# Kernel tuning notes

Measured on AMD Instinct MI355X. Metric: run time of the kernel, lower is better.

The kernel has to match this reference:

```python
import jax, jax.numpy as jnp
import numpy as np
from jax import lax

B, D, C, K = 8192, 512, 1000, 8
EPS = 1e-8
TEMP = 0.2
NEG = -10000.0


def setup_inputs() -> dict:
    key = jax.random.key(0)
    ks = jax.random.split(key, 6)
    z = jax.random.normal(ks[0], (B, D), dtype=jnp.float32)
    n_exp = jax.random.randint(ks[1], (B,), 0, K, dtype=jnp.int32)
    s1 = 1.0 / np.sqrt(D)
    W1 = jax.random.normal(ks[2], (K, D, D), dtype=jnp.float32) * s1
    b1 = jax.random.normal(ks[3], (K, D), dtype=jnp.float32) * 0.01
    W2 = jax.random.normal(ks[4], (K, D, C), dtype=jnp.float32) * s1
    b2 = jax.random.normal(ks[5], (K, C), dtype=jnp.float32) * 0.01
    return {"z": z, "n_exp": n_exp, "W1": W1, "b1": b1, "W2": W2, "b2": b2}


def _gates_one(p, c, n):
    # p: [K,C] softmax probs for one sample; c: [K] confidences; n: scalar int
    pn = p / (jnp.linalg.norm(p, axis=-1, keepdims=True) + EPS)
    S = pn @ pn.T  # [K,K] pairwise cosine similarity
    sel0 = jnp.zeros((K,), dtype=bool).at[jnp.argmax(c)].set(True)

    def body(t, sel):
        # max cosine sim of each candidate to already-selected set
        max_sim = jnp.max(jnp.where(sel[None, :], S, -jnp.inf), axis=1)
        dist = jnp.where(sel, -jnp.inf, 1.0 - max_sim)
        new = sel.at[jnp.argmax(dist)].set(True)
        return jnp.where(t < n, new, sel)

    sel = lax.fori_loop(1, K, body, sel0)
    gate_logits = jnp.where(sel, c, NEG) / TEMP
    return jax.nn.softmax(gate_logits)


def reference(z, n_exp, W1, b1, W2, b2):
    # K expert MLPs, batched: [B,d] -> [B,K,C]
    h = jax.nn.relu(jnp.einsum('bd,kde->bke', z, W1) + b1[None])
    logits_all = jnp.einsum('bke,kec->bkc', h, W2) + b2[None]
    probs = jax.nn.softmax(logits_all, axis=-1)
    conf = jnp.max(probs, axis=-1)  # [B,K]
    gates = jax.vmap(_gates_one)(probs, conf, n_exp)  # [B,K]
    logits = jnp.einsum('bkc,bk->bc', logits_all, gates)
    return logits, gates
```

## Files before the change

kernel.cpp:

```cpp
#include <hip/hip_runtime.h>
#include <math.h>

#define B_SZ 8192
#define D_DIM 512
#define C_DIM 1000
#define C_PAD 1024
#define K_EXP 8
#define TEMP_INV 5.0f
#define EPS_N 1e-8f

typedef __attribute__((ext_vector_type(8))) short frag_ab;
typedef __attribute__((ext_vector_type(16))) float f32x16;

__device__ __forceinline__ short f2bf(float f) {
    unsigned u = __builtin_bit_cast(unsigned, f);
    unsigned r = (u + 0x7fffu + ((u >> 16) & 1u)) >> 16;
    return (short)r;
}
__device__ __forceinline__ float bf2f(short s) {
    unsigned u = ((unsigned)(unsigned short)s) << 16;
    return __builtin_bit_cast(float, u);
}
__device__ __forceinline__ void split2(float v, short& s0, short& s1) {
    s0 = f2bf(v);
    s1 = f2bf(v - bf2f(s0));
}

__device__ __forceinline__ void gl_lds16(const short* g, short* l) {
    __builtin_amdgcn_global_load_lds(
        (const __attribute__((address_space(1))) unsigned int*)(const void*)g,
        (__attribute__((address_space(3))) unsigned int*)(void*)l,
        16, 0, 0);
}

__global__ __launch_bounds__(256) void prep_z(const float* __restrict__ z,
                                              short* __restrict__ p0, short* __restrict__ p1) {
    int idx = blockIdx.x * 256 + threadIdx.x;
    float v = z[idx];
    short a, b; split2(v, a, b);
    p0[idx] = a; p1[idx] = b;
}

__global__ __launch_bounds__(256) void prep_w1t(const float* __restrict__ W1,
                                                short* __restrict__ p0, short* __restrict__ p1) {
    __shared__ float t[32][33];
    const int k = blockIdx.z;
    const int d0 = blockIdx.x * 32;
    const int e0 = blockIdx.y * 32;
    const int tx = threadIdx.x & 31, ty = threadIdx.x >> 5;
    const float* src = W1 + ((size_t)k << 18);
#pragma unroll
    for (int r = 0; r < 4; r++) {
        int d = d0 + ty + 8 * r;
        t[ty + 8 * r][tx] = src[(size_t)d * 512 + e0 + tx];
    }
    __syncthreads();
#pragma unroll
    for (int r = 0; r < 4; r++) {
        int e = e0 + ty + 8 * r;
        int d = d0 + tx;
        float v = t[tx][ty + 8 * r];
        short a, b; split2(v, a, b);
        size_t o = ((size_t)k << 18) + (size_t)e * 512 + d;
        p0[o] = a; p1[o] = b;
    }
}

__global__ __launch_bounds__(256) void prep_w2t(const float* __restrict__ W2,
                                                short* __restrict__ p0, short* __restrict__ p1) {
    __shared__ float t[32][33];
    const int k = blockIdx.z;
    const int e0 = blockIdx.x * 32;
    const int c0 = blockIdx.y * 32;
    const int tx = threadIdx.x & 31, ty = threadIdx.x >> 5;
    const float* src = W2 + (size_t)k * (D_DIM * C_DIM);
#pragma unroll
    for (int r = 0; r < 4; r++) {
        int e = e0 + ty + 8 * r;
        int c = c0 + tx;
        t[ty + 8 * r][tx] = (c < C_DIM) ? src[(size_t)e * C_DIM + c] : 0.f;
    }
    __syncthreads();
#pragma unroll
    for (int r = 0; r < 4; r++) {
        int c = c0 + ty + 8 * r;
        int e = e0 + tx;
        float v = t[tx][ty + 8 * r];
        short a, b; split2(v, a, b);
        size_t o = (size_t)k * (C_PAD * D_DIM) + (size_t)c * 512 + e;
        p0[o] = a; p1[o] = b;
    }
}

__global__ __launch_bounds__(512, 2) void gemm_split(
    const short* __restrict__ A0, const short* __restrict__ A1, long long aBatch,
    const short* __restrict__ B0, const short* __restrict__ B1, long long bBatch,
    const float* __restrict__ bias, int biasBatch,
    float* __restrict__ Cf, long long cBatch, int ldc, int Nout,
    short* __restrict__ H0, short* __restrict__ H1, long long hBatch,
    int mt, int nt, int mode)
{
    const int lin = blockIdx.x;
    const int k = lin & 7;
    const int rem = lin >> 3;
    const int gm = (mt >= 2) ? 2 : 1;
    const int win = rem / (gm * nt);
    const int local = rem % (gm * nt);
    const int m0 = (win * gm + local / nt) * 256;
    const int n0 = (local % nt) * 256;

    const int tid = threadIdx.x;
    const int lane = tid & 63;
    const int wv = tid >> 6;
    const int wm = (wv & 1) * 128;
    const int wn = (wv >> 1) * 64;

    __shared__ short lds[65536];
    short* ldsA = lds;
    short* ldsB = lds + 32768;

    const short* aP0 = A0 + (size_t)k * aBatch + (size_t)m0 * 512;
    const short* aP1 = A1 + (size_t)k * aBatch + (size_t)m0 * 512;
    const short* bP0 = B0 + (size_t)k * bBatch + (size_t)n0 * 512;
    const short* bP1 = B1 + (size_t)k * bBatch + (size_t)n0 * 512;

    f32x16 acc[4][2];
#pragma unroll
    for (int i = 0; i < 4; i++)
#pragma unroll
        for (int j = 0; j < 2; j++)
            acc[i][j] = (f32x16)(0.f);

    const int srow = tid >> 2;
    const int sc   = tid & 3;
    const int khalf = lane >> 5;
    const int r31   = lane & 31;

#define SROW_STAGE(gsrc, ldst, KK0) do {                                        \
    _Pragma("unroll")                                                           \
    for (int hh = 0; hh < 2; hh++) {                                            \
        int row = hh * 128 + srow;                                              \
        int gq = sc ^ ((row >> 1) & 3);                                         \
        gl_lds16((gsrc) + (size_t)row * 512 + (KK0) + gq * 8,                   \
                 (ldst) + row * 32 + sc * 8);                                   \
    }                                                                           \
} while (0)

#define READ_B32(BUFC) do {                                                     \
    _Pragma("unroll")                                                           \
    for (int p = 0; p < 2; p++)                                                 \
        _Pragma("unroll")                                                       \
        for (int bj = 0; bj < 2; bj++) {                                        \
            int R = wn + bj * 32 + r31;                                         \
            _Pragma("unroll")                                                   \
            for (int kk = 0; kk < 2; kk++) {                                    \
                int ck = kk * 2 + khalf;                                        \
                int slot = ck ^ ((R >> 1) & 3);                                 \
                bfr[p][bj][kk] = *(const frag_ab*)(ldsB + (BUFC) + p * 8192 + R * 32 + slot * 8); \
            }                                                                   \
        }                                                                       \
} while (0)

#define READ_A32(DST, BLK, BUFC) do {                                           \
    int R = wm + (BLK) * 32 + r31;                                              \
    _Pragma("unroll")                                                           \
    for (int p = 0; p < 2; p++)                                                 \
        _Pragma("unroll")                                                       \
        for (int kk = 0; kk < 2; kk++) {                                        \
            int ck = kk * 2 + khalf;                                            \
            int slot = ck ^ ((R >> 1) & 3);                                     \
            DST[p][kk] = *(const frag_ab*)(ldsA + (BUFC) + p * 8192 + R * 32 + slot * 8); \
        }                                                                       \
} while (0)

#define MFMA_Q32(BLK, AR) do {                                                  \
    __builtin_amdgcn_s_setprio(1);                                              \
    _Pragma("unroll")                                                           \
    for (int bj = 0; bj < 2; bj++) {                                            \
        f32x16 c = acc[BLK][bj];                                                \
        _Pragma("unroll")                                                       \
        for (int kk = 0; kk < 2; kk++) {                                        \
            c = __builtin_amdgcn_mfma_f32_32x32x16_bf16(AR[0][kk], bfr[0][bj][kk], c, 0, 0, 0); \
            c = __builtin_amdgcn_mfma_f32_32x32x16_bf16(AR[0][kk], bfr[1][bj][kk], c, 0, 0, 0); \
            c = __builtin_amdgcn_mfma_f32_32x32x16_bf16(AR[1][kk], bfr[0][bj][kk], c, 0, 0, 0); \
        }                                                                       \
        acc[BLK][bj] = c;                                                       \
    }                                                                           \
    __builtin_amdgcn_s_setprio(0);                                              \
} while (0)

#define PH_BAR() do {                                                           \
    __builtin_amdgcn_sched_barrier(0);                                          \
    __builtin_amdgcn_s_barrier();                                               \
    __builtin_amdgcn_sched_barrier(0);                                          \
} while (0)

    SROW_STAGE(bP0, ldsB + 0,            0);
    SROW_STAGE(bP1, ldsB + 8192,         0);
    SROW_STAGE(aP0, ldsA + 0,            0);
    SROW_STAGE(aP1, ldsA + 8192,         0);
    SROW_STAGE(bP0, ldsB + 16384,        32);
    SROW_STAGE(bP1, ldsB + 16384 + 8192, 32);
    asm volatile("s_waitcnt vmcnt(4)" ::: "memory");
    PH_BAR();

    auto kstep = [&](int T, bool s01, bool s23, int vmn) __attribute__((always_inline)) {
        const int bufc = (T & 1) * 16384;
        const int nb1  = ((T + 1) & 1) * 16384;
        const int kk1  = (T + 1) * 32;
        const int kk2  = (T + 2) * 32;
        frag_ab bfr[2][2][2];
        frag_ab aC[2][2], aN[2][2];

        READ_B32(bufc);
        READ_A32(aC, 0, bufc);
        READ_A32(aN, 1, bufc);
        if (s01) SROW_STAGE(aP0, ldsA + nb1, kk1);
        MFMA_Q32(0, aC);
        PH_BAR();

        READ_A32(aC, 2, bufc);
        if (s01) SROW_STAGE(aP1, ldsA + nb1 + 8192, kk1);
        MFMA_Q32(1, aN);
        PH_BAR();

        READ_A32(aN, 3, bufc);
        if (s23) SROW_STAGE(bP0, ldsB + bufc, kk2);
        MFMA_Q32(2, aC);
        PH_BAR();

        if (s23) SROW_STAGE(bP1, ldsB + bufc + 8192, kk2);
        MFMA_Q32(3, aN);
        if (vmn == 4)      asm volatile("s_waitcnt vmcnt(4)" ::: "memory");
        else if (vmn == 0) asm volatile("s_waitcnt vmcnt(0)" ::: "memory");
        PH_BAR();
    };

    for (int t = 0; t < 14; ++t) kstep(t, true, true, 4);
    kstep(14, true, false, 0);
    kstep(15, false, false, -1);

#undef SROW_STAGE
#undef READ_B32
#undef READ_A32
#undef MFMA_Q32
#undef PH_BAR

    const int er0 = (lane >> 5) * 4;
    const int ec  = lane & 31;
    if (mode == 0) {
        float* C = Cf + (size_t)k * cBatch;
        const float* bb = bias + (size_t)k * biasBatch;
#pragma unroll
        for (int blk = 0; blk < 4; blk++) {
            int rowb = m0 + wm + blk * 32 + er0;
#pragma unroll
            for (int bj = 0; bj < 2; bj++) {
                int col = n0 + wn + bj * 32 + ec;
                if (col < Nout) {
                    float b = bb[col];
#pragma unroll
                    for (int rg = 0; rg < 16; rg++) {
                        int row = rowb + (rg & 3) + 8 * (rg >> 2);
                        C[(size_t)row * ldc + col] = acc[blk][bj][rg] + b;
                    }
                }
            }
        }
    } else {
        short* h0 = H0 + (size_t)k * hBatch;
        short* h1 = H1 + (size_t)k * hBatch;
        const float* bb = bias + (size_t)k * biasBatch;
#pragma unroll
        for (int blk = 0; blk < 4; blk++) {
            int rowb = m0 + wm + blk * 32 + er0;
#pragma unroll
            for (int bj = 0; bj < 2; bj++) {
                int col = n0 + wn + bj * 32 + ec;
                float b = bb[col];
#pragma unroll
                for (int rg = 0; rg < 16; rg++) {
                    int row = rowb + (rg & 3) + 8 * (rg >> 2);
                    float v = fmaxf(acc[blk][bj][rg] + b, 0.f);
                    short s0, s1; split2(v, s0, s1);
                    size_t o = (size_t)row * 512 + col;
                    h0[o] = s0; h1[o] = s1;
                }
            }
        }
    }
}

__global__ __launch_bounds__(256) void gate_combine(
    const float* __restrict__ L,
    const int* __restrict__ n_exp,
    float* __restrict__ out_logits,
    float* __restrict__ out_gates,
    int Bc)
{
    const int wv = threadIdx.x >> 6;
    const int lane = threadIdx.x & 63;
    const int b = blockIdx.x * 4 + wv;
    const size_t kcs = (size_t)Bc * C_DIM;
    const float* Lb = L + (size_t)b * C_DIM;

    __shared__ float Sm[4][64];
    __shared__ float Zm[4][8];

    float mx[K_EXP], Zs[K_EXP], dd[36];
#pragma unroll
    for (int k = 0; k < K_EXP; k++) { mx[k] = -INFINITY; Zs[k] = 0.f; }
#pragma unroll
    for (int p = 0; p < 36; p++) dd[p] = 0.f;

    for (int c = lane; c < C_DIM; c += 64) {
        float e[K_EXP];
#pragma unroll
        for (int k = 0; k < K_EXP; k++) {
            float l = Lb[(size_t)k * kcs + c];
            mx[k] = fmaxf(mx[k], l);
            e[k] = __expf(l);
            Zs[k] += e[k];
        }
        int idx = 0;
#pragma unroll
        for (int i = 0; i < K_EXP; i++)
#pragma unroll
            for (int j = i; j < K_EXP; j++) {
                dd[idx] = fmaf(e[i], e[j], dd[idx]);
                idx++;
            }
    }

#pragma unroll
    for (int off = 32; off > 0; off >>= 1) {
#pragma unroll
        for (int k = 0; k < K_EXP; k++) {
            mx[k] = fmaxf(mx[k], __shfl_xor(mx[k], off, 64));
            Zs[k] += __shfl_xor(Zs[k], off, 64);
        }
#pragma unroll
        for (int p = 0; p < 36; p++)
            dd[p] += __shfl_xor(dd[p], off, 64);
    }

    if (lane == 0) {
        int idx = 0;
#pragma unroll
        for (int i = 0; i < K_EXP; i++)
#pragma unroll
            for (int j = i; j < K_EXP; j++) {
                Sm[wv][i * 8 + j] = dd[idx];
                Sm[wv][j * 8 + i] = dd[idx];
                idx++;
            }
#pragma unroll
        for (int k = 0; k < K_EXP; k++) Zm[wv][k] = Zs[k];
    }

    const int ti = lane >> 3, tj = lane & 7;
    const float Zi = Zm[wv][ti], Zj = Zm[wv][tj];
    const float dij = Sm[wv][ti * 8 + tj];
    const float dii = Sm[wv][ti * 8 + ti];
    const float djj = Sm[wv][tj * 8 + tj];
    const float ni = sqrtf(dii) / Zi + EPS_N;
    const float nj = sqrtf(djj) / Zj + EPS_N;
    const float cosij = (dij / (Zi * Zj)) / (ni * nj);

    float conf[K_EXP];
#pragma unroll
    for (int k = 0; k < K_EXP; k++) conf[k] = __expf(mx[k]) / Zs[k];

    int i0 = 0; float bcf = conf[0];
#pragma unroll
    for (int k = 1; k < K_EXP; k++)
        if (conf[k] > bcf) { bcf = conf[k]; i0 = k; }
    unsigned sel = 1u << i0;
    const int n = n_exp[b];

    for (int t = 1; t < K_EXP; t++) {
        float v = ((sel >> tj) & 1u) ? cosij : -INFINITY;
        v = fmaxf(v, __shfl_xor(v, 1, 64));
        v = fmaxf(v, __shfl_xor(v, 2, 64));
        v = fmaxf(v, __shfl_xor(v, 4, 64));
        float dist = ((sel >> ti) & 1u) ? -INFINITY : 1.0f - v;
        float bv = dist; int bi = ti;
#pragma unroll
        for (int off = 8; off < 64; off <<= 1) {
            float ov = __shfl_xor(bv, off, 64);
            int oi = __shfl_xor(bi, off, 64);
            if (ov > bv || (ov == bv && oi < bi)) { bv = ov; bi = oi; }
        }
        if (t < n) sel |= 1u << bi;
    }

    float cmax = -INFINITY;
#pragma unroll
    for (int k = 0; k < K_EXP; k++)
        if ((sel >> k) & 1u) cmax = fmaxf(cmax, conf[k]);
    float g[K_EXP], gsum = 0.f;
#pragma unroll
    for (int k = 0; k < K_EXP; k++) {
        g[k] = ((sel >> k) & 1u) ? __expf((conf[k] - cmax) * TEMP_INV) : 0.f;
        gsum += g[k];
    }
    const float ginv = 1.0f / gsum;
#pragma unroll
    for (int k = 0; k < K_EXP; k++) g[k] *= ginv;

    if (lane == 0) {
        float4* og = (float4*)(out_gates + (size_t)b * K_EXP);
        og[0] = make_float4(g[0], g[1], g[2], g[3]);
        og[1] = make_float4(g[4], g[5], g[6], g[7]);
    }

    for (int c = lane; c < C_DIM; c += 64) {
        float o = 0.f;
#pragma unroll
        for (int k = 0; k < K_EXP; k++)
            o = fmaf(g[k], Lb[(size_t)k * kcs + c], o);
        out_logits[(size_t)b * C_DIM + c] = o;
    }
}

extern "C" void kernel_launch(void* const* d_in, const int* in_sizes, int n_in,
                              void* d_out, int out_size, void* d_ws, size_t ws_size,
                              hipStream_t stream) {
    const float* z     = (const float*)d_in[0];
    const int*   n_exp = (const int*)d_in[1];
    const float* W1    = (const float*)d_in[2];
    const float* b1    = (const float*)d_in[3];
    const float* W2    = (const float*)d_in[4];
    const float* b2    = (const float*)d_in[5];
    float* out_logits = (float*)d_out;
    float* out_gates  = (float*)d_out + (size_t)B_SZ * C_DIM;

    const size_t zP   = (size_t)B_SZ * D_DIM * 2;
    const size_t w1P  = (size_t)K_EXP * D_DIM * D_DIM * 2;
    const size_t w2P  = (size_t)K_EXP * C_PAD * D_DIM * 2;
    const size_t fixedBytes = 2 * (zP + w1P + w2P);

    int nch = 1;
    while (nch < 32 && fixedBytes + (size_t)(B_SZ / nch) * 48384 > ws_size) nch *= 2;
    const int Bc = B_SZ / nch;

    char* w = (char*)d_ws;
    short* zp[2];  zp[0]  = (short*)w; zp[1]  = (short*)(w + zP);  w += 2 * zP;
    short* w1t[2]; w1t[0] = (short*)w; w1t[1] = (short*)(w + w1P); w += 2 * w1P;
    short* w2t[2]; w2t[0] = (short*)w; w2t[1] = (short*)(w + w2P); w += 2 * w2P;
    const size_t hP = (size_t)K_EXP * Bc * D_DIM * 2;
    short* hp[2];  hp[0]  = (short*)w; hp[1]  = (short*)(w + hP);  w += 2 * hP;
    float* Lb = (float*)w;

    prep_z <<<dim3((B_SZ * D_DIM) / 256), 256, 0, stream>>>(z, zp[0], zp[1]);
    prep_w1t<<<dim3(16, 16, K_EXP), 256, 0, stream>>>(W1, w1t[0], w1t[1]);
    prep_w2t<<<dim3(16, 32, K_EXP), 256, 0, stream>>>(W2, w2t[0], w2t[1]);

    const int mt = Bc / 256;

    for (int ch = 0; ch < nch; ch++) {
        const int off = ch * Bc;
        const long long zoff = (long long)off * D_DIM;

        gemm_split<<<dim3(8 * mt * 2), 512, 0, stream>>>(
            zp[0] + zoff, zp[1] + zoff, 0LL,
            w1t[0], w1t[1], (long long)D_DIM * D_DIM,
            b1, D_DIM,
            nullptr, 0LL, 0, D_DIM,
            hp[0], hp[1], (long long)Bc * D_DIM,
            mt, 2, 1);

        gemm_split<<<dim3(8 * mt * 4), 512, 0, stream>>>(
            hp[0], hp[1], (long long)Bc * D_DIM,
            w2t[0], w2t[1], (long long)C_PAD * D_DIM,
            b2, C_DIM,
            Lb, (long long)Bc * C_DIM, C_DIM, C_DIM,
            nullptr, nullptr, 0LL,
            mt, 4, 0);

        gate_combine<<<dim3(Bc / 4), 256, 0, stream>>>(
            Lb, n_exp + off,
            out_logits + (size_t)off * C_DIM,
            out_gates + (size_t)off * K_EXP,
            Bc);
    }
}
```

Measured before the change: 519.9 us.

## Store GEMM operands in 16x8 tiled global layout for contiguous LDS staging

Changes the bf16 split operand buffers (z, transposed W1, W2, and hidden H) from row-major to a tiled layout of 16-row by 8-column blocks. Global-to-LDS staging can then copy contiguous 1KB chunks per wave without the XOR swizzle, and LDS fragment reads index the tiled layout directly. The aim is better global load coalescing and fewer LDS bank conflicts. The trade-off is scattered stores in the prep and epilogue writes, and LDS reads now depend on the unswizzled tiled pattern avoiding conflicts.

Result: no change. 517.6 us (-0.5%).

```diff
diff --git a/kernel.cpp b/kernel.cpp
--- a/kernel.cpp
+++ b/kernel.cpp
@@ -33,12 +33,18 @@
         16, 0, 0);
 }
 
+__device__ __forceinline__ size_t tiled_off(int row, int k) {
+    return (size_t)(row >> 4) * 8192 + (size_t)(k >> 3) * 128 + (row & 15) * 8 + (k & 7);
+}
+
 __global__ __launch_bounds__(256) void prep_z(const float* __restrict__ z,
                                               short* __restrict__ p0, short* __restrict__ p1) {
     int idx = blockIdx.x * 256 + threadIdx.x;
+    int b = idx >> 9, d = idx & 511;
     float v = z[idx];
-    short a, b; split2(v, a, b);
-    p0[idx] = a; p1[idx] = b;
+    short a, bb; split2(v, a, bb);
+    size_t o = tiled_off(b, d);
+    p0[o] = a; p1[o] = bb;
 }
 
 __global__ __launch_bounds__(256) void prep_w1t(const float* __restrict__ W1,
@@ -61,7 +67,7 @@
         int d = d0 + tx;
         float v = t[tx][ty + 8 * r];
         short a, b; split2(v, a, b);
-        size_t o = ((size_t)k << 18) + (size_t)e * 512 + d;
+        size_t o = ((size_t)k << 18) + tiled_off(e, d);
         p0[o] = a; p1[o] = b;
     }
 }
@@ -87,7 +93,7 @@
         int e = e0 + tx;
         float v = t[tx][ty + 8 * r];
         short a, b; split2(v, a, b);
-        size_t o = (size_t)k * (C_PAD * D_DIM) + (size_t)c * 512 + e;
+        size_t o = (size_t)k * (C_PAD * D_DIM) + tiled_off(c, e);
         p0[o] = a; p1[o] = b;
     }
 }
@@ -131,18 +137,18 @@
         for (int j = 0; j < 2; j++)
             acc[i][j] = (f32x16)(0.f);
 
-    const int srow = tid >> 2;
-    const int sc   = tid & 3;
     const int khalf = lane >> 5;
     const int r31   = lane & 31;
+    const int lq    = lane >> 4;
+    const int l16   = lane & 15;
 
 #define SROW_STAGE(gsrc, ldst, KK0) do {                                        \
+    const int c0_ = (KK0) >> 3;                                                 \
     _Pragma("unroll")                                                           \
     for (int hh = 0; hh < 2; hh++) {                                            \
-        int row = hh * 128 + srow;                                              \
-        int gq = sc ^ ((row >> 1) & 3);                                         \
-        gl_lds16((gsrc) + (size_t)row * 512 + (KK0) + gq * 8,                   \
-                 (ldst) + row * 32 + sc * 8);                                   \
+        int rt = hh * 8 + wv;                                                   \
+        gl_lds16((gsrc) + (size_t)rt * 8192 + (size_t)(c0_ + lq) * 128 + l16 * 8, \
+                 (ldst) + rt * 512 + lane * 8);                                 \
     }                                                                           \
 } while (0)
 
@@ -152,24 +158,24 @@
         _Pragma("unroll")                                                       \
         for (int bj = 0; bj < 2; bj++) {                                        \
             int R = wn + bj * 32 + r31;                                         \
+            int rt = R >> 4, rm = R & 15;                                       \
             _Pragma("unroll")                                                   \
             for (int kk = 0; kk < 2; kk++) {                                    \
                 int ck = kk * 2 + khalf;                                        \
-                int slot = ck ^ ((R >> 1) & 3);                                 \
-                bfr[p][bj][kk] = *(const frag_ab*)(ldsB + (BUFC) + p * 8192 + R * 32 + slot * 8); \
+                bfr[p][bj][kk] = *(const frag_ab*)(ldsB + (BUFC) + p * 8192 + rt * 512 + ck * 128 + rm * 8); \
             }                                                                   \
         }                                                                       \
 } while (0)
 
 #define READ_A32(DST, BLK, BUFC) do {                                           \
     int R = wm + (BLK) * 32 + r31;                                              \
+    int rt = R >> 4, rm = R & 15;                                               \
     _Pragma("unroll")                                                           \
     for (int p = 0; p < 2; p++)                                                 \
         _Pragma("unroll")                                                       \
         for (int kk = 0; kk < 2; kk++) {                                        \
             int ck = kk * 2 + khalf;                                            \
-            int slot = ck ^ ((R >> 1) & 3);                                     \
-            DST[p][kk] = *(const frag_ab*)(ldsA + (BUFC) + p * 8192 + R * 32 + slot * 8); \
+            DST[p][kk] = *(const frag_ab*)(ldsA + (BUFC) + p * 8192 + rt * 512 + ck * 128 + rm * 8); \
         }                                                                       \
 } while (0)
 
@@ -283,7 +289,7 @@
                     int row = rowb + (rg & 3) + 8 * (rg >> 2);
                     float v = fmaxf(acc[blk][bj][rg] + b, 0.f);
                     short s0, s1; split2(v, s0, s1);
-                    size_t o = (size_t)row * 512 + col;
+                    size_t o = tiled_off(row, col);
                     h0[o] = s0; h1[o] = s1;
                 }
             }
```
